# Kernel optimization log

Hardware: AMD Instinct MI355X
Metric: run time of the kernel (lower is better)

The kernel has to match this reference:

```python
import jax, jax.numpy as jnp
import numpy as np

B, T, V, H = 128, 1024, 256, 512  # batch, max seq len, vocab_count, latent_dim
PAD_VALUE = 0.0  # pad_index = 0 used as padding_value in pad_packed_sequence


def setup_inputs() -> dict:
    key = jax.random.key(0)
    k_x, k_len, k_wi, k_wh, k_bi, k_bh = jax.random.split(key, 6)
    x = jax.random.randint(k_x, (B, T), 0, V, dtype=jnp.int32)
    x_len = jax.random.randint(k_len, (B,), 1, T + 1, dtype=jnp.int32)
    x_len = x_len.at[0].set(T)  # ensure padded output length == T (static shape)
    s = 0.05
    W_ih = jax.random.normal(k_wi, (4 * H, V), dtype=jnp.float32) * s
    W_hh = jax.random.normal(k_wh, (4 * H, H), dtype=jnp.float32) * s
    b_ih = jax.random.normal(k_bi, (4 * H,), dtype=jnp.float32) * s
    b_hh = jax.random.normal(k_bh, (4 * H,), dtype=jnp.float32) * s
    return {"x": x, "x_len": x_len, "W_ih": W_ih, "W_hh": W_hh,
            "b_ih": b_ih, "b_hh": b_hh}


def _lstm_packed(x, x_len, W_ih, W_hh, b_ih, b_hh):
    # one-hot input projection (mathematically == embedding gather W_ih.T[x])
    oh = jax.nn.one_hot(x, W_ih.shape[1], dtype=W_ih.dtype)          # [B,T,V]
    proj = jnp.einsum('btv,gv->btg', oh, W_ih) + b_ih + b_hh         # [B,T,4H]
    proj_t = jnp.transpose(proj, (1, 0, 2))                          # [T,B,4H]
    # mask[t,b] = True while t < x_len[b] (packed-sequence semantics)
    mask_t = jnp.arange(proj.shape[1])[:, None] < x_len[None, :]     # [T,B]

    h0 = jnp.zeros((x.shape[0], W_hh.shape[1]), dtype=W_ih.dtype)
    c0 = jnp.zeros_like(h0)

    def step(carry, inp):
        h, c = carry
        p, m = inp                                                   # [B,4H],[B]
        gates = p + h @ W_hh.T
        i, f, g, o = jnp.split(gates, 4, axis=-1)                    # torch order i,f,g,o
        i = jax.nn.sigmoid(i)
        f = jax.nn.sigmoid(f)
        g = jnp.tanh(g)
        o = jax.nn.sigmoid(o)
        c_new = f * c + i * g
        h_new = o * jnp.tanh(c_new)
        m1 = m[:, None]
        h = jnp.where(m1, h_new, h)   # freeze state past each sequence's length
        c = jnp.where(m1, c_new, c)
        out = jnp.where(m1, h_new, PAD_VALUE)  # padding_value = pad_index
        return (h, c), out

    (h_T, c_T), ys = jax.lax.scan(step, (h0, c0), (proj_t, mask_t))
    output = jnp.transpose(ys, (1, 0, 2))                            # [B,T,H]
    return output, h_T, c_T


def reference(x, x_len, W_ih, W_hh, b_ih, b_hh):
    output, h_T, c_T = _lstm_packed(x, x_len, W_ih, W_hh, b_ih, b_hh)
    # hidden/cell shaped [num_layers*num_dirs=1, B, H] like torch LSTM
    return output, h_T[None], c_T[None]
```

## Files before the change

kernel.cpp:

```cpp
#include <hip/hip_runtime.h>
#include <hip/hip_bf16.h>


#define TT 1024
#define BB 128
#define HH 512
#define VV 256
#define NGP 8
#define GM 16
#define NWG 8
#define NE 64
#define FSTRIDE 32

typedef __attribute__((ext_vector_type(8))) short short8;
typedef __attribute__((ext_vector_type(4))) float f32x4;
typedef unsigned long long u64;
typedef unsigned short u16;

__device__ __forceinline__ u16 f2bf(float f) {
  __hip_bfloat16 h = __float2bfloat16(f);
  return *reinterpret_cast<u16*>(&h);
}
__device__ __forceinline__ float sigm(float x) { return 1.0f / (1.0f + __expf(-x)); }
__device__ __forceinline__ float tanh_(float x) { return 1.0f - 2.0f / (1.0f + __expf(2.0f * x)); }

__global__ void lstm_init(const int* __restrict__ x, int* __restrict__ x_t,
                          unsigned int* __restrict__ hbuf0, int* __restrict__ flags) {
  int idx = blockIdx.x * 256 + threadIdx.x;
  int t = idx >> 7, b = idx & 127;
  x_t[idx] = x[b * TT + t];
  if (idx < (BB * HH / 2)) hbuf0[idx] = 0u;
  if (idx < NGP * NWG * FSTRIDE) flags[idx] = 0;
}

__launch_bounds__(256, 1)
__global__ void lstm_persist(const int* __restrict__ x_t, const int* __restrict__ x_len,
                             const float* __restrict__ W_ih, const float* __restrict__ W_hh,
                             const float* __restrict__ b_ih, const float* __restrict__ b_hh,
                             float* __restrict__ out,
                             u16* __restrict__ hbuf,
                             int* __restrict__ flags) {
  const int tid = threadIdx.x;
  const int wave = tid >> 6, lane = tid & 63;
  const int nn = lane & 15, quad = lane >> 4;
  const int g = blockIdx.x >> 3, ig = blockIdx.x & 7;

  __shared__ u16 hA[GM * 520];
  __shared__ float gates_s[GM * 260];
  __shared__ int gmax_s;

  short8 bw[4][16];
#pragma unroll
  for (int s = 0; s < 4; s++) {
    const float* src = W_hh + (size_t)(wave * HH + ig * NE + s * 16 + nn) * HH + quad * 8;
#pragma unroll
    for (int kt = 0; kt < 16; kt++) {
      const float* p = src + kt * 32;
      short8 v;
#pragma unroll
      for (int j = 0; j < 8; j++) v[j] = (short)f2bf(p[j]);
      bw[s][kt] = v;
    }
  }

  const int bc = tid >> 4, e4 = (tid & 15) * 4;
  const int bglob = g * GM + bc;
  const int xl = x_len[bglob];
  float bias[4][4];
#pragma unroll
  for (int q = 0; q < 4; q++)
#pragma unroll
    for (int j = 0; j < 4; j++) {
      int grow = q * HH + ig * NE + e4 + j;
      bias[q][j] = b_ih[grow] + b_hh[grow];
    }
  float cst[4] = {0.f, 0.f, 0.f, 0.f}, hst[4] = {0.f, 0.f, 0.f, 0.f};

  if (tid == 0) gmax_s = 1;
  __syncthreads();
  if ((tid & 15) == 0) atomicMax(&gmax_s, xl);

  const int srow = tid >> 4, sc16 = tid & 15;
  const u64 stage_off = (u64)((size_t)(g * GM + srow) * HH * 2 + (size_t)sc16 * 16);

  int* flmine = flags + (g * NWG + ig) * FSTRIDE;

  __syncthreads();
  const int gmax = gmax_s;

  for (int t = 0; t < gmax; ++t) {
    const int slot = t & 1;

    const int xv = x_t[t * BB + bglob];
    float w[4][4];
#pragma unroll
    for (int q = 0; q < 4; q++)
#pragma unroll
      for (int j = 0; j < 4; j++)
        w[q][j] = W_ih[(size_t)(q * HH + ig * NE + e4 + j) * VV + xv];

    if (lane < 8 && lane != ig) {
      const int* fp = flags + (g * NWG + lane) * FSTRIDE;
      while (__hip_atomic_load(fp, __ATOMIC_RELAXED, __HIP_MEMORY_SCOPE_AGENT) < t)
        __builtin_amdgcn_s_sleep(1);
    }

    {
      u64 gsrc = (u64)(hbuf + (size_t)slot * (BB * HH)) + stage_off;
      short8 t0, t1, t2, t3;
      asm volatile(
          "global_load_dwordx4 %0, %4, off sc1\n\t"
          "global_load_dwordx4 %1, %4, off offset:256 sc1\n\t"
          "global_load_dwordx4 %2, %4, off offset:512 sc1\n\t"
          "global_load_dwordx4 %3, %4, off offset:768 sc1\n\t"
          "s_waitcnt vmcnt(0)"
          : "=&v"(t0), "=&v"(t1), "=&v"(t2), "=&v"(t3)
          : "v"(gsrc)
          : "memory");
      short8* dst = (short8*)(hA + srow * 520 + sc16 * 8);
      dst[0] = t0; dst[16] = t1; dst[32] = t2; dst[48] = t3;
    }
    __syncthreads();

    {
      f32x4 acc[4] = {{0,0,0,0},{0,0,0,0},{0,0,0,0},{0,0,0,0}};
      const u16* ap = hA + nn * 520 + quad * 8;
#pragma unroll
      for (int kt = 0; kt < 16; kt++) {
        short8 a = *(const short8*)(ap + kt * 32);
#pragma unroll
        for (int s = 0; s < 4; s++)
          acc[s] = __builtin_amdgcn_mfma_f32_16x16x32_bf16(a, bw[s][kt], acc[s], 0, 0, 0);
      }
#pragma unroll
      for (int s = 0; s < 4; s++)
#pragma unroll
        for (int r = 0; r < 4; r++)
          gates_s[(quad * 4 + r) * 260 + wave * NE + s * 16 + nn] = acc[s][r];
    }
    __syncthreads();

    {
      f32x4 G0 = *(const f32x4*)&gates_s[bc * 260 + 0 * NE + e4];
      f32x4 G1 = *(const f32x4*)&gates_s[bc * 260 + 1 * NE + e4];
      f32x4 G2 = *(const f32x4*)&gates_s[bc * 260 + 2 * NE + e4];
      f32x4 G3 = *(const f32x4*)&gates_s[bc * 260 + 3 * NE + e4];
      const bool act = (t < xl);
      f32x4 outv;
#pragma unroll
      for (int j = 0; j < 4; j++) {
        float gi = G0[j] + w[0][j] + bias[0][j];
        float gf = G1[j] + w[1][j] + bias[1][j];
        float gg = G2[j] + w[2][j] + bias[2][j];
        float go = G3[j] + w[3][j] + bias[3][j];
        float iv = sigm(gi), fv = sigm(gf), gv = tanh_(gg), ov = sigm(go);
        float cn = fv * cst[j] + iv * gv;
        float hn = ov * tanh_(cn);
        if (act) { cst[j] = cn; hst[j] = hn; }
        outv[j] = act ? hn : 0.0f;
      }
      u64 hword = (u64)f2bf(hst[0]) | ((u64)f2bf(hst[1]) << 16)
                | ((u64)f2bf(hst[2]) << 32) | ((u64)f2bf(hst[3]) << 48);
      u64* hdst = (u64*)(hbuf + (size_t)(slot ^ 1) * (BB * HH)
                         + (size_t)bglob * HH + ig * NE + e4);
      __hip_atomic_store(hdst, hword, __ATOMIC_RELAXED, __HIP_MEMORY_SCOPE_AGENT);
      asm volatile("s_waitcnt vmcnt(0)" ::: "memory");
      __builtin_nontemporal_store(outv,
          (f32x4*)&out[((size_t)bglob * TT + t) * HH + ig * NE + e4]);
    }
    __syncthreads();

    if (tid == 0)
      __hip_atomic_store(flmine, t + 1, __ATOMIC_RELAXED, __HIP_MEMORY_SCOPE_AGENT);
  }

  {
    f32x4 z = {0.f, 0.f, 0.f, 0.f};
    for (int t = gmax; t < TT; ++t)
      __builtin_nontemporal_store(z,
          (f32x4*)&out[((size_t)bglob * TT + t) * HH + ig * NE + e4]);
  }

  {
    f32x4 hv, cv;
#pragma unroll
    for (int j = 0; j < 4; j++) { hv[j] = hst[j]; cv[j] = cst[j]; }
    *(f32x4*)&out[(size_t)BB * TT * HH + (size_t)bglob * HH + ig * NE + e4] = hv;
    *(f32x4*)&out[(size_t)BB * TT * HH + (size_t)BB * HH + (size_t)bglob * HH + ig * NE + e4] = cv;
  }
}

extern "C" void kernel_launch(void* const* d_in, const int* in_sizes, int n_in,
                              void* d_out, int out_size, void* d_ws, size_t ws_size,
                              hipStream_t stream) {
  const int*   x     = (const int*)d_in[0];
  const int*   x_len = (const int*)d_in[1];
  const float* W_ih  = (const float*)d_in[2];
  const float* W_hh  = (const float*)d_in[3];
  const float* b_ih  = (const float*)d_in[4];
  const float* b_hh  = (const float*)d_in[5];
  float* out = (float*)d_out;

  char* ws = (char*)d_ws;
  int* x_t = (int*)ws;
  u16* hbuf = (u16*)(ws + 524288);
  int* flags = (int*)(ws + 524288 + 262144);

  lstm_init<<<512, 256, 0, stream>>>(x, x_t, (unsigned int*)hbuf, flags);
  lstm_persist<<<64, 256, 0, stream>>>(x_t, x_len, W_ih, W_hh, b_ih, b_hh, out, hbuf, flags);
}
```

Before: 5.436 ms.

## Replace flag-based inter-workgroup sync with step-tagged hidden-state packets

Drops the separate per-workgroup flag array and the spin on it. Each thread now publishes its bf16 hidden values interleaved with the step counter in one 16-byte store. Consumers poll the packets directly, reloading any chunk whose tags are stale, which removes the store-wait, an extra barrier and the flag round trip from every recurrent step. It also folds the bias into the gathered input weights and shrinks token storage to bytes. This doubles the hidden-buffer traffic and relies on 16-byte stores being observed atomically.

```diff
diff --git a/kernel.cpp b/kernel.cpp
--- a/kernel.cpp
+++ b/kernel.cpp
@@ -10,12 +10,14 @@
 #define GM 16
 #define NWG 8
 #define NE 64
-#define FSTRIDE 32
 
 typedef __attribute__((ext_vector_type(8))) short short8;
 typedef __attribute__((ext_vector_type(4))) float f32x4;
+typedef __attribute__((ext_vector_type(4))) unsigned u32x4;
 typedef unsigned long long u64;
 typedef unsigned short u16;
+typedef unsigned char u8;
+typedef unsigned u32;
 
 __device__ __forceinline__ u16 f2bf(float f) {
   __hip_bfloat16 h = __float2bfloat16(f);
@@ -24,22 +26,20 @@
 __device__ __forceinline__ float sigm(float x) { return 1.0f / (1.0f + __expf(-x)); }
 __device__ __forceinline__ float tanh_(float x) { return 1.0f - 2.0f / (1.0f + __expf(2.0f * x)); }
 
-__global__ void lstm_init(const int* __restrict__ x, int* __restrict__ x_t,
-                          unsigned int* __restrict__ hbuf0, int* __restrict__ flags) {
+__global__ void lstm_init(const int* __restrict__ x, u8* __restrict__ x_t,
+                          u32* __restrict__ hbuf) {
   int idx = blockIdx.x * 256 + threadIdx.x;
   int t = idx >> 7, b = idx & 127;
-  x_t[idx] = x[b * TT + t];
-  if (idx < (BB * HH / 2)) hbuf0[idx] = 0u;
-  if (idx < NGP * NWG * FSTRIDE) flags[idx] = 0;
+  x_t[idx] = (u8)x[b * TT + t];
+  hbuf[idx] = 0u;
 }
 
 __launch_bounds__(256, 1)
-__global__ void lstm_persist(const int* __restrict__ x_t, const int* __restrict__ x_len,
+__global__ void lstm_persist(const u8* __restrict__ x_t, const int* __restrict__ x_len,
                              const float* __restrict__ W_ih, const float* __restrict__ W_hh,
                              const float* __restrict__ b_ih, const float* __restrict__ b_hh,
                              float* __restrict__ out,
-                             u16* __restrict__ hbuf,
-                             int* __restrict__ flags) {
+                             u32* __restrict__ hbuf) {
   const int tid = threadIdx.x;
   const int wave = tid >> 6, lane = tid & 63;
   const int nn = lane & 15, quad = lane >> 4;
@@ -81,9 +81,10 @@
   if ((tid & 15) == 0) atomicMax(&gmax_s, xl);
 
   const int srow = tid >> 4, sc16 = tid & 15;
-  const u64 stage_off = (u64)((size_t)(g * GM + srow) * HH * 2 + (size_t)sc16 * 16);
-
-  int* flmine = flags + (g * NWG + ig) * FSTRIDE;
+  const u64 hb = (u64)hbuf;
+  const u64 crow_off = (u64)((size_t)(g * GM + srow) * 128 * 16);
+
+  const u64 pub_off = (u64)(((size_t)bglob * 128 + ig * 16 + (tid & 15)) * 16);
 
   __syncthreads();
   const int gmax = gmax_s;
@@ -91,34 +92,38 @@
   for (int t = 0; t < gmax; ++t) {
     const int slot = t & 1;
 
-    const int xv = x_t[t * BB + bglob];
+    const int xv = (int)x_t[t * BB + bglob];
     float w[4][4];
 #pragma unroll
     for (int q = 0; q < 4; q++)
 #pragma unroll
       for (int j = 0; j < 4; j++)
-        w[q][j] = W_ih[(size_t)(q * HH + ig * NE + e4 + j) * VV + xv];
-
-    if (lane < 8 && lane != ig) {
-      const int* fp = flags + (g * NWG + lane) * FSTRIDE;
-      while (__hip_atomic_load(fp, __ATOMIC_RELAXED, __HIP_MEMORY_SCOPE_AGENT) < t)
-        __builtin_amdgcn_s_sleep(1);
-    }
+        w[q][j] = W_ih[(size_t)(q * HH + ig * NE + e4 + j) * VV + xv] + bias[q][j];
 
     {
-      u64 gsrc = (u64)(hbuf + (size_t)slot * (BB * HH)) + stage_off;
-      short8 t0, t1, t2, t3;
-      asm volatile(
-          "global_load_dwordx4 %0, %4, off sc1\n\t"
-          "global_load_dwordx4 %1, %4, off offset:256 sc1\n\t"
-          "global_load_dwordx4 %2, %4, off offset:512 sc1\n\t"
-          "global_load_dwordx4 %3, %4, off offset:768 sc1\n\t"
-          "s_waitcnt vmcnt(0)"
-          : "=&v"(t0), "=&v"(t1), "=&v"(t2), "=&v"(t3)
-          : "v"(gsrc)
-          : "memory");
-      short8* dst = (short8*)(hA + srow * 520 + sc16 * 8);
-      dst[0] = t0; dst[16] = t1; dst[32] = t2; dst[48] = t3;
+      const u64 rb = hb + (u64)((size_t)slot * BB * 128 * 16) + crow_off;
+      u32x4 vv[8];
+      unsigned need = 0xFFu;
+      const unsigned tt = (unsigned)t;
+      while (need) {
+#pragma unroll
+        for (int k = 0; k < 8; ++k)
+          if (need & (1u << k)) {
+            asm volatile("global_load_dwordx4 %0, %1, off sc1"
+                         : "=v"(vv[k])
+                         : "v"(rb + (u64)((k * 16 + sc16) * 16))
+                         : "memory");
+          }
+        asm volatile("s_waitcnt vmcnt(0)" ::: "memory");
+#pragma unroll
+        for (int k = 0; k < 8; ++k)
+          if (vv[k][1] >= tt && vv[k][3] >= tt) need &= ~(1u << k);
+      }
+#pragma unroll
+      for (int k = 0; k < 8; ++k) {
+        u64 hw = (u64)vv[k][0] | ((u64)vv[k][2] << 32);
+        *reinterpret_cast<u64*>(&hA[srow * 520 + k * 64 + sc16 * 4]) = hw;
+      }
     }
     __syncthreads();
 
@@ -149,29 +154,27 @@
       f32x4 outv;
 #pragma unroll
       for (int j = 0; j < 4; j++) {
-        float gi = G0[j] + w[0][j] + bias[0][j];
-        float gf = G1[j] + w[1][j] + bias[1][j];
-        float gg = G2[j] + w[2][j] + bias[2][j];
-        float go = G3[j] + w[3][j] + bias[3][j];
+        float gi = G0[j] + w[0][j];
+        float gf = G1[j] + w[1][j];
+        float gg = G2[j] + w[2][j];
+        float go = G3[j] + w[3][j];
         float iv = sigm(gi), fv = sigm(gf), gv = tanh_(gg), ov = sigm(go);
         float cn = fv * cst[j] + iv * gv;
         float hn = ov * tanh_(cn);
         if (act) { cst[j] = cn; hst[j] = hn; }
         outv[j] = act ? hn : 0.0f;
       }
-      u64 hword = (u64)f2bf(hst[0]) | ((u64)f2bf(hst[1]) << 16)
-                | ((u64)f2bf(hst[2]) << 32) | ((u64)f2bf(hst[3]) << 48);
-      u64* hdst = (u64*)(hbuf + (size_t)(slot ^ 1) * (BB * HH)
-                         + (size_t)bglob * HH + ig * NE + e4);
-      __hip_atomic_store(hdst, hword, __ATOMIC_RELAXED, __HIP_MEMORY_SCOPE_AGENT);
-      asm volatile("s_waitcnt vmcnt(0)" ::: "memory");
       __builtin_nontemporal_store(outv,
           (f32x4*)&out[((size_t)bglob * TT + t) * HH + ig * NE + e4]);
-    }
-    __syncthreads();
-
-    if (tid == 0)
-      __hip_atomic_store(flmine, t + 1, __ATOMIC_RELAXED, __HIP_MEMORY_SCOPE_AGENT);
+      u32x4 pub;
+      pub[0] = (u32)f2bf(hst[0]) | ((u32)f2bf(hst[1]) << 16);
+      pub[1] = (u32)(t + 1);
+      pub[2] = (u32)f2bf(hst[2]) | ((u32)f2bf(hst[3]) << 16);
+      pub[3] = (u32)(t + 1);
+      u64 pa = hb + (u64)((size_t)(slot ^ 1) * BB * 128 * 16) + pub_off;
+      asm volatile("global_store_dwordx4 %0, %1, off sc1"
+                   :: "v"(pa), "v"(pub) : "memory");
+    }
   }
 
   {
@@ -202,10 +205,9 @@
   float* out = (float*)d_out;
 
   char* ws = (char*)d_ws;
-  int* x_t = (int*)ws;
-  u16* hbuf = (u16*)(ws + 524288);
-  int* flags = (int*)(ws + 524288 + 262144);
-
-  lstm_init<<<512, 256, 0, stream>>>(x, x_t, (unsigned int*)hbuf, flags);
-  lstm_persist<<<64, 256, 0, stream>>>(x_t, x_len, W_ih, W_hh, b_ih, b_hh, out, hbuf, flags);
-}
+  u8*  x_t  = (u8*)ws;
+  u32* hbuf = (u32*)(ws + 131072);
+
+  lstm_init<<<512, 256, 0, stream>>>(x, x_t, hbuf);
+  lstm_persist<<<64, 256, 0, stream>>>(x_t, x_len, W_ih, W_hh, b_ih, b_hh, out, hbuf);
+}
```

Measured after the change: 5.462 ms. About the same (+0.5%).
